# Kernel tuning notes

Measured on AMD Instinct MI355X. Metric: run time of the kernel, lower is better.

## Reference

```python
import jax, jax.numpy as jnp
import numpy as np

K = 5            # kernel_size
MAX_ORIENT = 8
MAX_LEVEL = 4
D = (K - 1) // 2  # pad amount = 2


def setup_inputs() -> dict:
    key = jax.random.key(0)
    k1, k2, k3 = jax.random.split(key, 3)
    x = jax.random.normal(k1, (32, 1, 512, 512), dtype=jnp.float32)
    fwd_f = jax.random.normal(k2, (MAX_ORIENT, 1, K, K), dtype=jnp.float32)
    fwd_f = fwd_f.at[0, 0].set(jnp.ones((K, K), dtype=jnp.float32))  # per __init__
    inv_f = jax.random.normal(k3, (MAX_ORIENT, 1, K, K), dtype=jnp.float32)
    return {"x": x, "forward_filters": fwd_f, "inverse_filters": inv_f}


def _pad_for_tconv(p):
    # faithful port of padding_for_transpose_conv (static python ints)
    ip, op = 0, 0
    if p > 0:
        op = p
    elif p < 0:
        a = -p
        if a % 2 == 0:
            ip = a // 2
        else:
            op = 1
            ip = (a + 1) // 2
    return ip, op


def _conv2d(x, w, stride, pad):
    # torch F.pad(x, (d,d,d,d)) then conv2d(stride) == conv with symmetric padding
    return jax.lax.conv_general_dilated(
        x, w, window_strides=(stride, stride),
        padding=((pad, pad), (pad, pad)),
        dimension_numbers=("NCHW", "OIHW", "NCHW"))


def _conv_transpose2d(x, w, stride, pad, out_pad):
    # torch conv_transpose2d, weight layout (in_ch, out_ch, kH, kW).
    # Equivalent direct conv: flip kernel spatially, swap I/O axes,
    # lhs_dilation=stride, padding lo=k-1-p, hi=k-1-p+output_padding.
    k = w.shape[2]
    w2 = jnp.transpose(jnp.flip(w, (2, 3)), (1, 0, 2, 3))  # OIHW (1,8,5,5)
    padding = tuple((k - 1 - p, k - 1 - p + op) for p, op in zip(pad, out_pad))
    return jax.lax.conv_general_dilated(
        x, w2, window_strides=(1, 1), padding=padding,
        lhs_dilation=(stride, stride),
        dimension_numbers=("NCHW", "OIHW", "NCHW"))


def _forward_transform(x, fwd_f):
    result = [None] * (MAX_LEVEL + 1)
    vimg = x
    level = MAX_LEVEL
    res = None
    while level > 0 and vimg.shape[2] > 1 and vimg.shape[3] > 1:
        res = _conv2d(vimg, fwd_f, 2, D)   # (B, 8, ceil(H/2)+?, ...)
        result[level] = res
        vimg = res[:, :1]                  # lowpass band feeds next level
        level -= 1
    result[0] = res[:, :1]
    return result


def _inverse_transform(coeffs, inp_dim, inv_f):
    rec = coeffs[0]
    for level in range(1, MAX_LEVEL + 1):
        cur = np.array(coeffs[level].shape[2:])
        target = np.array(inp_dim) if level == MAX_LEVEL else np.array(coeffs[level + 1].shape[2:])
        pc = target - 2 * (cur - 1) - K
        ip0, op0 = _pad_for_tconv(int(pc[0]))
        ip1, op1 = _pad_for_tconv(int(pc[1]))
        full = jnp.concatenate([rec, coeffs[level][:, 1:]], axis=1)  # (B,8,h,w)
        rec = _conv_transpose2d(full, inv_f, 2, (ip0, ip1), (op0, op1))
    return rec


def reference(x, forward_filters, inverse_filters):
    coeffs = _forward_transform(x, forward_filters)
    return _inverse_transform(coeffs, x.shape[2:], inverse_filters)
```

## Files before the change

### kernel.cpp

```cpp
#include <hip/hip_runtime.h>

#define NORIENT 8

__device__ __forceinline__ unsigned xcd_swz(unsigned bid, unsigned nwg) {
    unsigned chunk = nwg >> 3;
    return (nwg & 7u) ? bid : (bid & 7u) * chunk + (bid >> 3);
}

__global__ void fwd_conv_wave_kernel(const float* __restrict__ in, long in_img_stride,
                                     const float* __restrict__ filt,
                                     float* __restrict__ out,
                                     int H, int W, int OH, int OW, int N) {
    constexpr int SROW = 104;
    __shared__ float tile[67 * SROW];

    int nbx = OW >> 5, nby = OH >> 5;
    unsigned sb = xcd_swz(blockIdx.x, gridDim.x);
    int bx = (int)(sb % nbx);
    unsigned t = sb / nbx;
    int by = (int)(t % nby);
    int n = (int)(t / nby);

    const float* __restrict__ ip = in + (long)n * in_img_stride;
    int tid = threadIdx.x;

    int w = __builtin_amdgcn_readfirstlane(tid >> 6);
    const float* __restrict__ F = filt + w * 25;
    float Wt[25];
#pragma unroll
    for (int k = 0; k < 25; ++k) Wt[k] = F[k];

    int gy0 = 64 * by - 2, gx0 = 64 * bx - 4;
#pragma unroll
    for (int k = 0; k < 3; ++k) {
        int e = tid + k * 512;
        if (e < 67 * 18) {
            int row = e / 18, m = e - row * 18;
            int gy = gy0 + row, gx = gx0 + 4 * m;
            bool vl = (gy >= 0) & (gy < H) & (gx >= 0) & (gx <= W - 4);
            float4 val = *(const float4*)(ip + (vl ? ((long)gy * W + gx) : 0));
            float msk = vl ? 1.f : 0.f;
            int off = row * SROW + 4 * m + 4 * (m >> 1);
            *(float4*)&tile[off] = make_float4(val.x * msk, val.y * msk,
                                               val.z * msk, val.w * msk);
        }
    }
    __syncthreads();

    int lane = tid & 63;
    int lx = lane & 7, ly = lane >> 3;

    float acc[4][4];
#pragma unroll
    for (int o = 0; o < 4; ++o)
#pragma unroll
        for (int dx = 0; dx < 4; ++dx) acc[o][dx] = 0.f;

#pragma unroll
    for (int r = 0; r < 11; ++r) {
        int base = (8 * ly + r) * SROW + 12 * lx;
        float2 A2 = *(const float2*)&tile[base + 2];
        float4 B  = *(const float4*)&tile[base + 4];
        float4 C  = *(const float4*)&tile[base + 12];
        float  D  = tile[base + 16];
        float Q[11] = {A2.x, A2.y, B.x, B.y, B.z, B.w, C.x, C.y, C.z, C.w, D};

#pragma unroll
        for (int o = 0; o < 4; ++o) {
            int i = r - 2 * o;
            if (i < 0 || i > 4) continue;
#pragma unroll
            for (int j = 0; j < 5; ++j) {
                float wv = Wt[i * 5 + j];
#pragma unroll
                for (int dx = 0; dx < 4; ++dx)
                    acc[o][dx] = fmaf(Q[2 * dx + j], wv, acc[o][dx]);
            }
        }
    }

    long cs = (long)OH * OW;
    int oy = 32 * by + 4 * ly, ox = 32 * bx + 4 * lx;
    long ob = ((long)n * NORIENT + w) * cs + (long)oy * OW + ox;
#pragma unroll
    for (int o = 0; o < 4; ++o)
        *(float4*)(out + ob + (long)o * OW) =
            make_float4(acc[o][0], acc[o][1], acc[o][2], acc[o][3]);
}

__global__ void fwd4_inv1_fused_kernel(const float* __restrict__ l2,
                                       const float* __restrict__ fwd_f,
                                       const float* __restrict__ inv_f,
                                       float* __restrict__ r1) {
    constexpr int SROW = 104;
    __shared__ float tile[67 * SROW];
    __shared__ float l1t[NORIENT * 32 * 32];

    int n = blockIdx.x;
    const float* __restrict__ ip = l2 + (long)n * 8 * 64 * 64;
    int tid = threadIdx.x;

    int w = __builtin_amdgcn_readfirstlane(tid >> 6);
    {
        const float* __restrict__ F = fwd_f + w * 25;
        float Wt[25];
#pragma unroll
        for (int k = 0; k < 25; ++k) Wt[k] = F[k];

#pragma unroll
        for (int k = 0; k < 3; ++k) {
            int e = tid + k * 512;
            if (e < 67 * 18) {
                int row = e / 18, m = e - row * 18;
                int gy = -2 + row, gx = -4 + 4 * m;
                bool vl = (gy >= 0) & (gy < 64) & (gx >= 0) & (gx <= 60);
                float4 val = *(const float4*)(ip + (vl ? ((long)gy * 64 + gx) : 0));
                float msk = vl ? 1.f : 0.f;
                int off = row * SROW + 4 * m + 4 * (m >> 1);
                *(float4*)&tile[off] = make_float4(val.x * msk, val.y * msk,
                                                   val.z * msk, val.w * msk);
            }
        }
        __syncthreads();

        int lane = tid & 63;
        int lx = lane & 7, ly = lane >> 3;

        float acc[4][4];
#pragma unroll
        for (int o = 0; o < 4; ++o)
#pragma unroll
            for (int dx = 0; dx < 4; ++dx) acc[o][dx] = 0.f;

#pragma unroll
        for (int r = 0; r < 11; ++r) {
            int base = (8 * ly + r) * SROW + 12 * lx;
            float2 A2 = *(const float2*)&tile[base + 2];
            float4 B  = *(const float4*)&tile[base + 4];
            float4 C  = *(const float4*)&tile[base + 12];
            float  D  = tile[base + 16];
            float Q[11] = {A2.x, A2.y, B.x, B.y, B.z, B.w, C.x, C.y, C.z, C.w, D};

#pragma unroll
            for (int o = 0; o < 4; ++o) {
                int i = r - 2 * o;
                if (i < 0 || i > 4) continue;
#pragma unroll
                for (int j = 0; j < 5; ++j) {
                    float wv = Wt[i * 5 + j];
#pragma unroll
                    for (int dx = 0; dx < 4; ++dx)
                        acc[o][dx] = fmaf(Q[2 * dx + j], wv, acc[o][dx]);
                }
            }
        }

#pragma unroll
        for (int o = 0; o < 4; ++o)
            *(float4*)&l1t[w * 1024 + (4 * ly + o) * 32 + 4 * lx] =
                make_float4(acc[o][0], acc[o][1], acc[o][2], acc[o][3]);
    }
    __syncthreads();

    if (tid < 256) {
        int b0 = tid & 15, a0 = tid >> 4;

        bool fmv = a0 > 0, fpv = a0 < 15;
        bool um = b0 > 0, up = b0 < 15;
        float fm = fmv ? 1.f : 0.f, fp_ = fpv ? 1.f : 0.f;
        int r0 = (fmv ? 2 * a0 - 1 : 0) * 32;
        int r1o = (2 * a0) * 32;
        int r2o = (2 * a0 + 1) * 32;
        int r3o = (fpv ? 2 * a0 + 2 : 2 * a0 + 1) * 32;
        int cL = um ? 2 * b0 - 2 : 0;
        int cM = 2 * b0;
        int cR = up ? 2 * b0 + 2 : 0;
        const int ro[4] = {r0, r1o, r2o, r3o};
        const float rm[4] = {fm, 1.f, 1.f, fp_};

        float acc[2][2][2][2];
#pragma unroll
        for (int i = 0; i < 2; ++i)
#pragma unroll
            for (int j = 0; j < 2; ++j)
#pragma unroll
                for (int k = 0; k < 2; ++k)
#pragma unroll
                    for (int l = 0; l < 2; ++l) acc[i][j][k][l] = 0.f;

#pragma unroll
        for (int c = 0; c < NORIENT; ++c) {
            const float* __restrict__ F = inv_f + c * 25;
            int coff = c * 1024;
            float P[4][4];
#pragma unroll
            for (int r = 0; r < 4; ++r) {
                int base = coff + ro[r];
                float2 L = *(const float2*)&l1t[base + cL];
                float2 M = *(const float2*)&l1t[base + cM];
                float2 R = *(const float2*)&l1t[base + cR];
                float mask = rm[r];
                P[r][0] = (um ? L.y : 0.f) * mask;
                P[r][1] = M.x * mask;
                P[r][2] = M.y * mask;
                P[r][3] = (up ? R.x : 0.f) * mask;
            }
#pragma unroll
            for (int a = 0; a < 3; ++a) {
#pragma unroll
                for (int b = 0; b < 3; ++b) {
                    float w00 = F[(4 - 2 * a) * 5 + (4 - 2 * b)];
                    float w01 = (b >= 1) ? F[(4 - 2 * a) * 5 + (5 - 2 * b)] : 0.f;
                    float w10 = (a >= 1) ? F[(5 - 2 * a) * 5 + (4 - 2 * b)] : 0.f;
                    float w11 = (a >= 1 && b >= 1) ? F[(5 - 2 * a) * 5 + (5 - 2 * b)] : 0.f;
#pragma unroll
                    for (int sr = 0; sr < 2; ++sr) {
#pragma unroll
                        for (int sc = 0; sc < 2; ++sc) {
                            float pv = P[sr + a][sc + b];
                            acc[sr][sc][0][0] = fmaf(pv, w00, acc[sr][sc][0][0]);
                            if (b >= 1) acc[sr][sc][0][1] = fmaf(pv, w01, acc[sr][sc][0][1]);
                            if (a >= 1) acc[sr][sc][1][0] = fmaf(pv, w10, acc[sr][sc][1][0]);
                            if (a >= 1 && b >= 1)
                                        acc[sr][sc][1][1] = fmaf(pv, w11, acc[sr][sc][1][1]);
                        }
                    }
                }
            }
        }

        long ob = (long)n * 4096 + (long)(4 * a0) * 64 + 4 * b0;
        *(float4*)(r1 + ob)       = make_float4(acc[0][0][0][0], acc[0][0][0][1],
                                                acc[0][1][0][0], acc[0][1][0][1]);
        *(float4*)(r1 + ob + 64)  = make_float4(acc[0][0][1][0], acc[0][0][1][1],
                                                acc[0][1][1][0], acc[0][1][1][1]);
        *(float4*)(r1 + ob + 128) = make_float4(acc[1][0][0][0], acc[1][0][0][1],
                                                acc[1][1][0][0], acc[1][1][0][1]);
        *(float4*)(r1 + ob + 192) = make_float4(acc[1][0][1][0], acc[1][0][1][1],
                                                acc[1][1][1][0], acc[1][1][1][1]);
    }
}

__global__ void inv_tconv_kernel(const float* __restrict__ rec, long rec_img_stride,
                                 const float* __restrict__ coef,
                                 const float* __restrict__ filt,
                                 float* __restrict__ out,
                                 int h, int w, int N) {
    int h2 = h >> 1, w2 = w >> 1;
    unsigned sb = xcd_swz(blockIdx.x, gridDim.x);
    long idx = (long)sb * blockDim.x + threadIdx.x;
    long total = (long)N * h2 * w2;
    if (idx >= total) return;
    int b0 = (int)(idx % w2);
    long t = idx / w2;
    int a0 = (int)(t % h2);
    int n = (int)(t / h2);

    const float* __restrict__ rp = rec + (long)n * rec_img_stride;
    const float* __restrict__ cp = coef + (long)n * (long)NORIENT * h * w;
    long cs = (long)h * w;

    bool fmv = a0 > 0, fpv = a0 < h2 - 1;
    bool um = b0 > 0, up = b0 < w2 - 1;
    float fm = fmv ? 1.f : 0.f, fp_ = fpv ? 1.f : 0.f;
    int r0 = (fmv ? 2 * a0 - 1 : 0) * w;
    int r1 = (2 * a0) * w;
    int r2 = (2 * a0 + 1) * w;
    int r3 = (fpv ? 2 * a0 + 2 : 2 * a0 + 1) * w;
    int am  = um ? 2 * b0 - 1 : 0;
    int bm2 = up ? 2 * b0 + 1 : w - 2;

    float acc[2][2][2][2];
#pragma unroll
    for (int i = 0; i < 2; ++i)
#pragma unroll
        for (int j = 0; j < 2; ++j)
#pragma unroll
            for (int k = 0; k < 2; ++k)
#pragma unroll
                for (int l = 0; l < 2; ++l) acc[i][j][k][l] = 0.f;

    auto do_channel = [&](const float* __restrict__ src, const float* __restrict__ F) {
        float P[4][4];
        const int ro[4] = {r0, r1, r2, r3};
        const float rm[4] = {fm, 1.f, 1.f, fp_};
#pragma unroll
        for (int r = 0; r < 4; ++r) {
            const float* base = src + ro[r];
            float2 X = *(const float2*)(base + am);
            float2 Y = *(const float2*)(base + bm2);
            float mask = rm[r];
            P[r][0] = (um ? X.x : 0.f) * mask;
            P[r][1] = (um ? X.y : X.x) * mask;
            P[r][2] = (up ? Y.x : Y.y) * mask;
            P[r][3] = (up ? Y.y : 0.f) * mask;
        }
#pragma unroll
        for (int a = 0; a < 3; ++a) {
#pragma unroll
            for (int b = 0; b < 3; ++b) {
                float w00 = F[(4 - 2 * a) * 5 + (4 - 2 * b)];
                float w01 = (b >= 1) ? F[(4 - 2 * a) * 5 + (5 - 2 * b)] : 0.f;
                float w10 = (a >= 1) ? F[(5 - 2 * a) * 5 + (4 - 2 * b)] : 0.f;
                float w11 = (a >= 1 && b >= 1) ? F[(5 - 2 * a) * 5 + (5 - 2 * b)] : 0.f;
#pragma unroll
                for (int sr = 0; sr < 2; ++sr) {
#pragma unroll
                    for (int sc = 0; sc < 2; ++sc) {
                        float pv = P[sr + a][sc + b];
                        acc[sr][sc][0][0] = fmaf(pv, w00, acc[sr][sc][0][0]);
                        if (b >= 1) acc[sr][sc][0][1] = fmaf(pv, w01, acc[sr][sc][0][1]);
                        if (a >= 1) acc[sr][sc][1][0] = fmaf(pv, w10, acc[sr][sc][1][0]);
                        if (a >= 1 && b >= 1)
                                    acc[sr][sc][1][1] = fmaf(pv, w11, acc[sr][sc][1][1]);
                    }
                }
            }
        }
    };

    do_channel(rp, filt);
#pragma unroll
    for (int c = 1; c < NORIENT; ++c)
        do_channel(cp + (long)c * cs, filt + c * 25);

    int OW = w << 1;
    long ob = (long)n * 4 * cs + (long)(4 * a0) * OW + 4 * b0;
    *(float4*)(out + ob)          = make_float4(acc[0][0][0][0], acc[0][0][0][1],
                                                acc[0][1][0][0], acc[0][1][0][1]);
    *(float4*)(out + ob + OW)     = make_float4(acc[0][0][1][0], acc[0][0][1][1],
                                                acc[0][1][1][0], acc[0][1][1][1]);
    *(float4*)(out + ob + 2 * OW) = make_float4(acc[1][0][0][0], acc[1][0][0][1],
                                                acc[1][1][0][0], acc[1][1][0][1]);
    *(float4*)(out + ob + 3 * OW) = make_float4(acc[1][0][1][0], acc[1][0][1][1],
                                                acc[1][1][1][0], acc[1][1][1][1]);
}

extern "C" void kernel_launch(void* const* d_in, const int* in_sizes, int n_in,
                              void* d_out, int out_size, void* d_ws, size_t ws_size,
                              hipStream_t stream) {
    const float* x     = (const float*)d_in[0];
    const float* fwd_f = (const float*)d_in[1];
    const float* inv_f = (const float*)d_in[2];
    float* out = (float*)d_out;
    float* ws  = (float*)d_ws;

    const int N = 32;

    float* l4 = ws;
    float* l3 = l4 + 16777216;
    float* l2 = l3 + 4194304;
    float* r1 = l2 + 1048576;
    float* r2 = r1 + 131072;
    float* r3 = r2 + 524288;

    dim3 blkF(512), blk(256);
    auto nblocks = [](long total) { return dim3((unsigned)((total + 255) / 256)); };

    fwd_conv_wave_kernel<<<dim3(32 * 8 * 8), blkF, 0, stream>>>(
        x, 512L * 512, fwd_f, l4, 512, 512, 256, 256, N);
    fwd_conv_wave_kernel<<<dim3(32 * 4 * 4), blkF, 0, stream>>>(
        l4, 8L * 256 * 256, fwd_f, l3, 256, 256, 128, 128, N);
    fwd_conv_wave_kernel<<<dim3(32 * 2 * 2), blkF, 0, stream>>>(
        l3, 8L * 128 * 128, fwd_f, l2, 128, 128, 64, 64, N);

    fwd4_inv1_fused_kernel<<<dim3(32), blkF, 0, stream>>>(l2, fwd_f, inv_f, r1);

    inv_tconv_kernel<<<nblocks(32L * 32 * 32), blk, 0, stream>>>(
        r1, 64L * 64, l2, inv_f, r2, 64, 64, N);
    inv_tconv_kernel<<<nblocks(32L * 64 * 64), blk, 0, stream>>>(
        r2, 128L * 128, l3, inv_f, r3, 128, 128, N);
    inv_tconv_kernel<<<nblocks(32L * 128 * 128), blk, 0, stream>>>(
        r3, 256L * 256, l4, inv_f, out, 256, 256, N);
}
```

Before: 96.08 us.

## Stage inverse transposed-conv input tiles into LDS via direct global-to-LDS loads

The inverse transposed-conv kernel becomes a tiled kernel. Each 256-thread block uses global_load_lds to copy a 16x32 input tile with halo, across all 8 channels, into shared memory. Each thread then produces a 2x4 output patch instead of 4x4, reading its neighbours from LDS instead of issuing redundant overlapping global loads. This cuts duplicated global/L2 traffic and uses asynchronous DMA-style loads, at the cost of a block-wide barrier, halves per-thread work, and uses clamped indices with masks at the borders.

```diff
diff --git a/kernel.cpp b/kernel.cpp
--- a/kernel.cpp
+++ b/kernel.cpp
@@ -241,60 +241,84 @@
     }
 }
 
-__global__ void inv_tconv_kernel(const float* __restrict__ rec, long rec_img_stride,
-                                 const float* __restrict__ coef,
-                                 const float* __restrict__ filt,
-                                 float* __restrict__ out,
-                                 int h, int w, int N) {
-    int h2 = h >> 1, w2 = w >> 1;
+__global__ void inv_tconv_dma_kernel(const float* __restrict__ rec, long rec_img_stride,
+                                     const float* __restrict__ coef,
+                                     const float* __restrict__ filt,
+                                     float* __restrict__ out,
+                                     int h, int w, int N) {
+    constexpr int SROW = 40;
+    constexpr int CH = 18 * SROW;
+    __shared__ float stage[6144];
+
+    int nbx = w >> 5, nby = h >> 4;
     unsigned sb = xcd_swz(blockIdx.x, gridDim.x);
-    long idx = (long)sb * blockDim.x + threadIdx.x;
-    long total = (long)N * h2 * w2;
-    if (idx >= total) return;
-    int b0 = (int)(idx % w2);
-    long t = idx / w2;
-    int a0 = (int)(t % h2);
-    int n = (int)(t / h2);
-
+    int bx = (int)(sb % nbx);
+    unsigned tt = sb / nbx;
+    int by = (int)(tt % nby);
+    int n = (int)(tt / nby);
+
+    int S0 = 16 * by, Q0 = 32 * bx;
+    long cs = (long)h * w;
     const float* __restrict__ rp = rec + (long)n * rec_img_stride;
-    const float* __restrict__ cp = coef + (long)n * (long)NORIENT * h * w;
-    long cs = (long)h * w;
-
-    bool fmv = a0 > 0, fpv = a0 < h2 - 1;
-    bool um = b0 > 0, up = b0 < w2 - 1;
-    float fm = fmv ? 1.f : 0.f, fp_ = fpv ? 1.f : 0.f;
-    int r0 = (fmv ? 2 * a0 - 1 : 0) * w;
-    int r1 = (2 * a0) * w;
-    int r2 = (2 * a0 + 1) * w;
-    int r3 = (fpv ? 2 * a0 + 2 : 2 * a0 + 1) * w;
-    int am  = um ? 2 * b0 - 1 : 0;
-    int bm2 = up ? 2 * b0 + 1 : w - 2;
-
-    float acc[2][2][2][2];
+    const float* __restrict__ cp = coef + (long)n * NORIENT * cs;
+
+    int tid = threadIdx.x;
+    int lane = tid & 63;
+    int wv = tid >> 6;
+
+#pragma unroll
+    for (int k = 0; k < 6; ++k) {
+        int fb = (wv * 6 + k) * 64;
+        int f = fb + lane;
+        int fc = (f < 1440) ? f : 1439;
+        int ch = fc / 180;
+        int rem = fc - ch * 180;
+        int row = rem / 10, m = rem - row * 10;
+        int gy = S0 - 1 + row;
+        gy = gy < 0 ? 0 : (gy >= h ? h - 1 : gy);
+        int gx = Q0 - 4 + 4 * m;
+        gx = gx < 0 ? 0 : (gx > w - 4 ? w - 4 : gx);
+        const float* __restrict__ src = ch ? (cp + (long)ch * cs) : rp;
+        __builtin_amdgcn_global_load_lds(src + (long)gy * w + gx,
+                                         &stage[(unsigned)f * 4], 16, 0, 0);
+    }
+    __syncthreads();
+
+    int sx = tid & 15, sy = tid >> 4;
+
+    float rm0 = (S0 + sy - 1 >= 0) ? 1.f : 0.f;
+    float rm2 = (S0 + sy + 1 < h) ? 1.f : 0.f;
+    float cm0 = (Q0 + 2 * sx - 1 >= 0) ? 1.f : 0.f;
+    float cm3 = (Q0 + 2 * sx + 2 < w) ? 1.f : 0.f;
+
+    float acc[2][2][2];
 #pragma unroll
     for (int i = 0; i < 2; ++i)
 #pragma unroll
-        for (int j = 0; j < 2; ++j)
-#pragma unroll
-            for (int k = 0; k < 2; ++k)
-#pragma unroll
-                for (int l = 0; l < 2; ++l) acc[i][j][k][l] = 0.f;
-
-    auto do_channel = [&](const float* __restrict__ src, const float* __restrict__ F) {
-        float P[4][4];
-        const int ro[4] = {r0, r1, r2, r3};
-        const float rm[4] = {fm, 1.f, 1.f, fp_};
-#pragma unroll
-        for (int r = 0; r < 4; ++r) {
-            const float* base = src + ro[r];
-            float2 X = *(const float2*)(base + am);
-            float2 Y = *(const float2*)(base + bm2);
-            float mask = rm[r];
-            P[r][0] = (um ? X.x : 0.f) * mask;
-            P[r][1] = (um ? X.y : X.x) * mask;
-            P[r][2] = (up ? Y.x : Y.y) * mask;
-            P[r][3] = (up ? Y.y : 0.f) * mask;
-        }
+        for (int j = 0; j < 2; ++j) {
+            acc[i][j][0] = 0.f;
+            acc[i][j][1] = 0.f;
+        }
+
+#pragma unroll
+    for (int c = 0; c < NORIENT; ++c) {
+        const float* __restrict__ F = filt + c * 25;
+        const float* __restrict__ tc = &stage[c * CH];
+
+        float P[3][4];
+#pragma unroll
+        for (int r = 0; r < 3; ++r) {
+            const float* rowp = tc + (sy + r) * SROW;
+            float2 L  = *(const float2*)(rowp + 2 * sx + 2);
+            float2 Fa = *(const float2*)(rowp + 2 * sx + 4);
+            float2 Fb = *(const float2*)(rowp + 2 * sx + 6);
+            float rmask = (r == 0) ? rm0 : ((r == 2) ? rm2 : 1.f);
+            P[r][0] = L.y  * rmask * cm0;
+            P[r][1] = Fa.x * rmask;
+            P[r][2] = Fa.y * rmask;
+            P[r][3] = Fb.x * rmask * cm3;
+        }
+
 #pragma unroll
         for (int a = 0; a < 3; ++a) {
 #pragma unroll
@@ -304,36 +328,24 @@
                 float w10 = (a >= 1) ? F[(5 - 2 * a) * 5 + (4 - 2 * b)] : 0.f;
                 float w11 = (a >= 1 && b >= 1) ? F[(5 - 2 * a) * 5 + (5 - 2 * b)] : 0.f;
 #pragma unroll
-                for (int sr = 0; sr < 2; ++sr) {
-#pragma unroll
-                    for (int sc = 0; sc < 2; ++sc) {
-                        float pv = P[sr + a][sc + b];
-                        acc[sr][sc][0][0] = fmaf(pv, w00, acc[sr][sc][0][0]);
-                        if (b >= 1) acc[sr][sc][0][1] = fmaf(pv, w01, acc[sr][sc][0][1]);
-                        if (a >= 1) acc[sr][sc][1][0] = fmaf(pv, w10, acc[sr][sc][1][0]);
-                        if (a >= 1 && b >= 1)
-                                    acc[sr][sc][1][1] = fmaf(pv, w11, acc[sr][sc][1][1]);
-                    }
+                for (int sc = 0; sc < 2; ++sc) {
+                    float pv = P[a][sc + b];
+                    acc[sc][0][0] = fmaf(pv, w00, acc[sc][0][0]);
+                    if (b >= 1) acc[sc][0][1] = fmaf(pv, w01, acc[sc][0][1]);
+                    if (a >= 1) acc[sc][1][0] = fmaf(pv, w10, acc[sc][1][0]);
+                    if (a >= 1 && b >= 1)
+                                acc[sc][1][1] = fmaf(pv, w11, acc[sc][1][1]);
                 }
             }
         }
-    };
-
-    do_channel(rp, filt);
-#pragma unroll
-    for (int c = 1; c < NORIENT; ++c)
-        do_channel(cp + (long)c * cs, filt + c * 25);
+    }
 
     int OW = w << 1;
-    long ob = (long)n * 4 * cs + (long)(4 * a0) * OW + 4 * b0;
-    *(float4*)(out + ob)          = make_float4(acc[0][0][0][0], acc[0][0][0][1],
-                                                acc[0][1][0][0], acc[0][1][0][1]);
-    *(float4*)(out + ob + OW)     = make_float4(acc[0][0][1][0], acc[0][0][1][1],
-                                                acc[0][1][1][0], acc[0][1][1][1]);
-    *(float4*)(out + ob + 2 * OW) = make_float4(acc[1][0][0][0], acc[1][0][0][1],
-                                                acc[1][1][0][0], acc[1][1][0][1]);
-    *(float4*)(out + ob + 3 * OW) = make_float4(acc[1][0][1][0], acc[1][0][1][1],
-                                                acc[1][1][1][0], acc[1][1][1][1]);
+    long ob = (long)n * 4 * cs + (long)(2 * (S0 + sy)) * OW + (2 * Q0 + 4 * sx);
+    *(float4*)(out + ob)      = make_float4(acc[0][0][0], acc[0][0][1],
+                                            acc[1][0][0], acc[1][0][1]);
+    *(float4*)(out + ob + OW) = make_float4(acc[0][1][0], acc[0][1][1],
+                                            acc[1][1][0], acc[1][1][1]);
 }
 
 extern "C" void kernel_launch(void* const* d_in, const int* in_sizes, int n_in,
@@ -355,7 +367,6 @@
     float* r3 = r2 + 524288;
 
     dim3 blkF(512), blk(256);
-    auto nblocks = [](long total) { return dim3((unsigned)((total + 255) / 256)); };
 
     fwd_conv_wave_kernel<<<dim3(32 * 8 * 8), blkF, 0, stream>>>(
         x, 512L * 512, fwd_f, l4, 512, 512, 256, 256, N);
@@ -366,10 +377,10 @@
 
     fwd4_inv1_fused_kernel<<<dim3(32), blkF, 0, stream>>>(l2, fwd_f, inv_f, r1);
 
-    inv_tconv_kernel<<<nblocks(32L * 32 * 32), blk, 0, stream>>>(
+    inv_tconv_dma_kernel<<<dim3(32 * 4 * 2), blk, 0, stream>>>(
         r1, 64L * 64, l2, inv_f, r2, 64, 64, N);
-    inv_tconv_kernel<<<nblocks(32L * 64 * 64), blk, 0, stream>>>(
+    inv_tconv_dma_kernel<<<dim3(32 * 8 * 4), blk, 0, stream>>>(
         r2, 128L * 128, l3, inv_f, r3, 128, 128, N);
-    inv_tconv_kernel<<<nblocks(32L * 128 * 128), blk, 0, stream>>>(
+    inv_tconv_dma_kernel<<<dim3(32 * 16 * 8), blk, 0, stream>>>(
         r3, 256L * 256, l4, inv_f, out, 256, 256, N);
 }
```

Result: faster. 91.00 us, median of 3 (-5.3%).
